# Kernel optimization log

Measured on AMD Instinct MI355X. Metric: run time of the kernel, lower is better.

The kernel has to match this reference:

```python
import jax, jax.numpy as jnp
import numpy as np

VIEW, NDET = 360, 736
H = W = 320
SCD, SDD = 500.0, 1000.0
DET_INT, REC_INT = 1.0, 1.1
NPOW2 = int(2 ** np.ceil(np.log2(2 * NDET - 1)))  # 2048
D_BETA = np.pi * 360.0 / VIEW / 180.0
DELTA_S = SCD / SDD * DET_INT


def _geometry():
    beta = np.linspace(0.0, (VIEW - 1) * D_BETA, VIEW)
    s_range = SCD / SDD * DET_INT * np.linspace((1 - NDET) / 2, (NDET - 1) / 2, NDET)
    cos_weight = np.cos(np.arctan2(s_range, SCD))
    # Ram-Lak spatial filter over offsets -(N-1)..(N-1), zero-padded to NPOW2, in freq domain
    n = np.arange(NPOW2) - (NDET - 1)
    h = np.zeros(NPOW2)
    h[n == 0] = 1.0 / (4.0 * DELTA_S ** 2)
    odd = (n % 2) != 0
    h[odd] = -1.0 / (np.pi * n[odd] * DELTA_S) ** 2
    recon_filter = np.real(np.fft.fft(h))[None, :]   # [1, NPOW2]
    window = np.ones((1, NPOW2))
    # backprojection sampling grid (fan-beam, equally spaced detector)
    x = REC_INT * np.linspace((1 - H) / 2, (H - 1) / 2, H)
    y = REC_INT * np.linspace((1 - W) / 2, (W - 1) / 2, W)
    x_mat, y_mat = np.meshgrid(x, y, indexing='xy')
    r = np.sqrt(x_mat ** 2 + y_mat ** 2)
    phi = np.arctan2(y_mat, x_mat)
    U = (SCD + r[None] * np.sin(beta[:, None, None] - phi[None])) / SCD
    s_xy = r[None] * np.cos(beta[:, None, None] - phi[None]) / U
    s_xy_n = (s_xy / s_range[-1]).reshape(VIEW, -1)
    view_xy_n = np.tile(np.linspace(-1.0, 1.0, VIEW)[:, None], [1, H * W])
    grid = np.stack([s_xy_n, view_xy_n], axis=2)     # [V, P, 2]
    square = (U ** 2).reshape(VIEW, -1)              # [V, P]
    # circular FOV mask
    gamma_e = np.arctan2(DET_INT * (NDET - 1) / 2, SDD)
    radius = SCD * np.sin(gamma_e) / REC_INT
    xg, yg = np.meshgrid(np.linspace(-(H - 1) / 2, (H - 1) / 2, H),
                         np.linspace(-(W - 1) / 2, (W - 1) / 2, W), indexing='xy')
    mask = ((((xg / radius) ** 2 + (yg / radius) ** 2) ** 2) < 1).astype(np.float32)
    return cos_weight, recon_filter, window, grid, square, mask


def setup_inputs() -> dict:
    key = jax.random.key(0)
    cw, rf, win, grid, square, mask = _geometry()
    f32 = lambda a: jnp.asarray(a, jnp.float32)
    return {
        "sinogram": jax.random.normal(key, (1, 1, VIEW, NDET), jnp.float32),
        "cos_weight": f32(cw), "recon_filter": f32(rf), "window": f32(win),
        "grid": f32(grid), "square": f32(square), "mask": f32(mask),
    }


def reference(sinogram, cos_weight, recon_filter, window, grid, square, mask):
    B, C, V, N = sinogram.shape
    Hh, Ww = mask.shape
    # FFT ramp filtering of cosine-weighted sinogram
    S = jnp.fft.fft(sinogram * cos_weight[None, None, None, :],
                    n=recon_filter.shape[-1], axis=-1)
    S = S * (recon_filter * window)[None, None]
    filt = (DELTA_S * jnp.fft.ifft(S, axis=-1)).real[..., N - 1:2 * N - 1]  # [B,C,V,N]
    # grid_sample: mode='nearest', padding_mode='zeros', align_corners=False
    gx, gy = grid[..., 0], grid[..., 1]                  # [V, P]
    ix = jnp.round(((gx + 1.0) * N - 1.0) / 2.0).astype(jnp.int32)
    iy = jnp.round(((gy + 1.0) * V - 1.0) / 2.0).astype(jnp.int32)
    valid = (ix >= 0) & (ix < N) & (iy >= 0) & (iy < V)
    sampled = filt[:, :, jnp.clip(iy, 0, V - 1), jnp.clip(ix, 0, N - 1)]   # [B,C,V,P]
    sampled = jnp.where(valid[None, None], sampled, 0.0)
    # weighted view-sum backprojection
    recon = D_BETA * jnp.sum(sampled / square[None, None], axis=2)         # [B,C,P]
    return recon.reshape(B, C, Hh, Ww) * mask[None, None]
```

## Files before the change

kernel.cpp:

```cpp
#include <hip/hip_runtime.h>

#define VIEWN 360
#define NDETC 736
#define HWPIX 102400
#define VC    8
#define VPC   45
#define NWORK 66240
#define FBLK  518

#define OFF_FILT 0
#define OFF_PART 1059840
#define OFF_DTAB 4336640
#define OFF_IY   4342400

__global__ __launch_bounds__(256) void filter_tab_kernel(
    const float* __restrict__ sino, const float* __restrict__ cw,
    const float* __restrict__ grid, char* __restrict__ ws)
{
    const int tid = threadIdx.x;
    if (blockIdx.x == FBLK) {
        double* dtab = (double*)(ws + OFF_DTAB);
        int*    iyt  = (int*)   (ws + OFF_IY);
        for (int v = tid; v < VIEWN; v += 256) {
            const double db   = ((3.141592653589793 * 360.0) / 360.0) / 180.0;
            const double stop = 359.0 * db;
            const double step = stop / 359.0;
            const double beta = (v == 359) ? stop : (double)v * step;
            dtab[2 * v]     = sin(beta);
            dtab[2 * v + 1] = cos(beta);
            const float gy = grid[(size_t)v * HWPIX * 2 + 1];
            float t = __fadd_rn(gy, 1.f);
            t = __fmul_rn(t, 360.f);
            t = __fadd_rn(t, -1.f);
            t = __fmul_rn(t, 0.5f);
            iyt[v] = __float2int_rn(t);
        }
        return;
    }
    __shared__ __align__(16) float gs[1472];
    __shared__ __align__(16) float ws2[2][NDETC];
    __shared__ __align__(16) float comb[128][4];
    float* filt = (float*)(ws + OFF_FILT);
    const int b = blockIdx.x;
    const int vbase = (b * 128) / 184;
    for (int m = tid; m < 1472; m += 256) {
        const int n1 = m - 735;
        const int n2 = ((2048 - m) & 2047) - 735;
        const double h1 = (n1 == 0) ? 1.0 : ((n1 & 1) ? -4.0 / (9.869604401089358 * (double)(n1 * n1)) : 0.0);
        const double h2 = (n2 == 0) ? 1.0 : ((n2 & 1) ? -4.0 / (9.869604401089358 * (double)(n2 * n2)) : 0.0);
        gs[m] = (float)(0.25 * (h1 + h2));
    }
    for (int idx = tid; idx < 2 * NDETC; idx += 256) {
        const int vv = idx / NDETC, k = idx % NDETC;
        const int v = vbase + vv;
        if (v < VIEWN) ws2[vv][k] = sino[v * NDETC + k] * cw[k];
    }
    __syncthreads();
    const int o    = b * 128 + (tid & 127);
    const int half = tid >> 7;
    float4 acc = make_float4(0.f, 0.f, 0.f, 0.f);
    int v = 0, d = 0;
    if (o < NWORK) {
        v = o / 184;
        d = 4 * (o % 184);
        const float* wsrow = ws2[v - vbase];
        const int kbeg = 368 * half;
        float4 p = *(const float4*)&gs[d + 736 - kbeg];
        for (int k0 = kbeg; k0 < kbeg + 368; k0 += 4) {
            const float4 c = *(const float4*)&gs[d + 732 - k0];
            const float4 w = *(const float4*)&wsrow[k0];
            acc.x = fmaf(w.x, c.w, acc.x);
            acc.y = fmaf(w.x, p.x, acc.y);
            acc.z = fmaf(w.x, p.y, acc.z);
            acc.w = fmaf(w.x, p.z, acc.w);
            acc.x = fmaf(w.y, c.z, acc.x);
            acc.y = fmaf(w.y, c.w, acc.y);
            acc.z = fmaf(w.y, p.x, acc.z);
            acc.w = fmaf(w.y, p.y, acc.w);
            acc.x = fmaf(w.z, c.y, acc.x);
            acc.y = fmaf(w.z, c.z, acc.y);
            acc.z = fmaf(w.z, c.w, acc.z);
            acc.w = fmaf(w.z, p.x, acc.w);
            acc.x = fmaf(w.w, c.x, acc.x);
            acc.y = fmaf(w.w, c.y, acc.y);
            acc.z = fmaf(w.w, c.z, acc.z);
            acc.w = fmaf(w.w, c.w, acc.w);
            p = c;
        }
    }
    if (half == 1) *(float4*)&comb[tid & 127][0] = acc;
    __syncthreads();
    if (half == 0 && o < NWORK) {
        const float4 bs = *(const float4*)&comb[tid][0];
        acc.x += bs.x; acc.y += bs.y; acc.z += bs.z; acc.w += bs.w;
        *(float4*)&filt[v * NDETC + d] = acc;
    }
}

__global__ __launch_bounds__(256) void bp_kernel(
    char* __restrict__ ws, float* __restrict__ part_out)
{
    const float*  filt = (const float*)(ws + OFF_FILT);
    const double* dtab = (const double*)(ws + OFF_DTAB);
    const int*    iyt  = (const int*)(ws + OFF_IY);
    const int pb = blockIdx.x, c = blockIdx.y;
    const int p  = pb * 256 + threadIdx.x;
    const int j  = p % 320, i = p / 320;
    const double xj = ((double)j - 159.5) * 1.1;
    const double yi = ((double)i - 159.5) * 1.1;
    const double CGX = 500.0 / 183.75;
    const double INV = 1.0 / 250000.0;
    float acc = 0.f;
    const int v0 = c * VPC;
    #pragma unroll 3
    for (int v = v0; v < v0 + VPC; ++v) {
        const double sb = dtab[2 * v];
        const double cb = dtab[2 * v + 1];
        const int iy = iyt[v];
        const double rs  = sb * xj - cb * yi;
        const double num = cb * xj + sb * yi;
        const double t   = 500.0 + rs;
        double r0 = (double)__builtin_amdgcn_rcpf((float)t);
        r0 = r0 * fma(-t, r0, 2.0);
        r0 = r0 * fma(-t, r0, 2.0);
        const double gxd = (num * CGX) * r0;
        const float  gx  = (float)gxd;
        float tx = __fadd_rn(gx, 1.f);
        tx = __fmul_rn(tx, 736.f);
        tx = __fadd_rn(tx, -1.f);
        tx = __fmul_rn(tx, 0.5f);
        const int ix = __float2int_rn(tx);
        const bool valid = (ix >= 0) & (ix < NDETC) & (iy >= 0) & (iy < VIEWN);
        const int ixc = min(max(ix, 0), NDETC - 1);
        const int iyc = min(max(iy, 0), VIEWN - 1);
        const float val = valid ? filt[iyc * NDETC + ixc] : 0.f;
        const float sq  = (float)(t * t * INV);
        acc += val * __builtin_amdgcn_rcpf(sq);
    }
    part_out[(size_t)c * HWPIX + p] = acc;
}

__global__ __launch_bounds__(256) void reduce_kernel(
    const float* __restrict__ part, const float* __restrict__ mask,
    float* __restrict__ out)
{
    const int p = blockIdx.x * 256 + threadIdx.x;
    const double db = ((3.141592653589793 * 360.0) / 360.0) / 180.0;
    float s = 0.f;
    #pragma unroll
    for (int cc = 0; cc < VC; ++cc)
        s += part[(size_t)cc * HWPIX + p];
    out[p] = (float)(db * (double)s * (double)mask[p]);
}

extern "C" void kernel_launch(void* const* d_in, const int* in_sizes, int n_in,
                              void* d_out, int out_size, void* d_ws, size_t ws_size,
                              hipStream_t stream)
{
    (void)in_sizes; (void)n_in; (void)out_size; (void)ws_size;
    const float* sino = (const float*)d_in[0];
    const float* cw   = (const float*)d_in[1];
    const float* grid = (const float*)d_in[4];
    const float* mask = (const float*)d_in[6];
    float* out = (float*)d_out;
    char*  ws  = (char*)d_ws;
    float* part = (float*)(ws + OFF_PART);

    filter_tab_kernel<<<FBLK + 1, 256, 0, stream>>>(sino, cw, grid, ws);
    bp_kernel<<<dim3(HWPIX / 256, VC), 256, 0, stream>>>(ws, part);
    reduce_kernel<<<HWPIX / 256, 256, 0, stream>>>(part, mask, out);
}
```

Measured before the change: 61.07 us.

## Compute backprojection coordinates in fp32 with wavefront-level fp64 fallback near rounding ties

The backprojection loop now computes the detector coordinate in fp32 from precomputed float sin/cos tables, including versions pre-scaled by the geometry constant. If any lane lands within a small margin of a rounding tie, the whole wavefront recomputes in fp64 so the nearest-neighbour index still matches the reference. The distance weight is derived from the fp32 reciprocal, views with an invalid row index are skipped, and the unroll factor changes. This targets the slow fp64 arithmetic, at the cost of a divergent fallback branch and slightly different fp32 weights.

```diff
diff --git a/kernel.cpp b/kernel.cpp
--- a/kernel.cpp
+++ b/kernel.cpp
@@ -11,7 +11,8 @@
 #define OFF_FILT 0
 #define OFF_PART 1059840
 #define OFF_DTAB 4336640
-#define OFF_IY   4342400
+#define OFF_FTAB 4348160
+#define OFF_IY   4353920
 
 __global__ __launch_bounds__(256) void filter_tab_kernel(
     const float* __restrict__ sino, const float* __restrict__ cw,
@@ -20,14 +21,18 @@
     const int tid = threadIdx.x;
     if (blockIdx.x == FBLK) {
         double* dtab = (double*)(ws + OFF_DTAB);
+        float*  ftab = (float*) (ws + OFF_FTAB);
         int*    iyt  = (int*)   (ws + OFF_IY);
         for (int v = tid; v < VIEWN; v += 256) {
             const double db   = ((3.141592653589793 * 360.0) / 360.0) / 180.0;
             const double stop = 359.0 * db;
             const double step = stop / 359.0;
             const double beta = (v == 359) ? stop : (double)v * step;
-            dtab[2 * v]     = sin(beta);
-            dtab[2 * v + 1] = cos(beta);
+            const double sb = sin(beta), cb = cos(beta);
+            const double CGX = 500.0 / 183.75;
+            dtab[4*v] = sb; dtab[4*v+1] = cb; dtab[4*v+2] = cb*CGX; dtab[4*v+3] = sb*CGX;
+            ftab[4*v] = (float)sb; ftab[4*v+1] = (float)cb;
+            ftab[4*v+2] = (float)(cb*CGX); ftab[4*v+3] = (float)(sb*CGX);
             const float gy = grid[(size_t)v * HWPIX * 2 + 1];
             float t = __fadd_rn(gy, 1.f);
             t = __fmul_rn(t, 360.f);
@@ -102,40 +107,49 @@
 {
     const float*  filt = (const float*)(ws + OFF_FILT);
     const double* dtab = (const double*)(ws + OFF_DTAB);
+    const float*  ftab = (const float*)(ws + OFF_FTAB);
     const int*    iyt  = (const int*)(ws + OFF_IY);
     const int pb = blockIdx.x, c = blockIdx.y;
     const int p  = pb * 256 + threadIdx.x;
     const int j  = p % 320, i = p / 320;
-    const double xj = ((double)j - 159.5) * 1.1;
-    const double yi = ((double)i - 159.5) * 1.1;
-    const double CGX = 500.0 / 183.75;
-    const double INV = 1.0 / 250000.0;
+    const float  xjf = ((float)j - 159.5f) * 1.1f;
+    const float  yif = ((float)i - 159.5f) * 1.1f;
+    const double xj  = ((double)j - 159.5) * 1.1;
+    const double yi  = ((double)i - 159.5) * 1.1;
     float acc = 0.f;
     const int v0 = c * VPC;
-    #pragma unroll 3
+    #pragma unroll 5
     for (int v = v0; v < v0 + VPC; ++v) {
-        const double sb = dtab[2 * v];
-        const double cb = dtab[2 * v + 1];
         const int iy = iyt[v];
-        const double rs  = sb * xj - cb * yi;
-        const double num = cb * xj + sb * yi;
-        const double t   = 500.0 + rs;
-        double r0 = (double)__builtin_amdgcn_rcpf((float)t);
-        r0 = r0 * fma(-t, r0, 2.0);
-        r0 = r0 * fma(-t, r0, 2.0);
-        const double gxd = (num * CGX) * r0;
-        const float  gx  = (float)gxd;
-        float tx = __fadd_rn(gx, 1.f);
+        if ((unsigned)iy >= 360u) continue;
+        const float sbf = ftab[4*v], cbf = ftab[4*v+1];
+        const float cbCf = ftab[4*v+2], sbCf = ftab[4*v+3];
+        const float t = fmaf(sbf, xjf, fmaf(-cbf, yif, 500.f));
+        const float r = __builtin_amdgcn_rcpf(t);
+        const float numC = fmaf(cbCf, xjf, sbCf * yif);
+        float tx = __fadd_rn(numC * r, 1.f);
         tx = __fmul_rn(tx, 736.f);
         tx = __fadd_rn(tx, -1.f);
         tx = __fmul_rn(tx, 0.5f);
+        const float dd = fabsf(tx - rintf(tx));
+        if (__any(dd > 0.499f)) {
+            const double sb = dtab[4*v], cb = dtab[4*v+1];
+            const double cbC = dtab[4*v+2], sbC = dtab[4*v+3];
+            const double td = fma(sb, xj, 500.0 - cb * yi);
+            double r0 = (double)__builtin_amdgcn_rcpf((float)td);
+            r0 = r0 * fma(-td, r0, 2.0);
+            r0 = r0 * fma(-td, r0, 2.0);
+            const double gxd = fma(cbC, xj, sbC * yi) * r0;
+            float txx = __fadd_rn((float)gxd, 1.f);
+            txx = __fmul_rn(txx, 736.f);
+            txx = __fadd_rn(txx, -1.f);
+            txx = __fmul_rn(txx, 0.5f);
+            tx = txx;
+        }
         const int ix = __float2int_rn(tx);
-        const bool valid = (ix >= 0) & (ix < NDETC) & (iy >= 0) & (iy < VIEWN);
-        const int ixc = min(max(ix, 0), NDETC - 1);
-        const int iyc = min(max(iy, 0), VIEWN - 1);
-        const float val = valid ? filt[iyc * NDETC + ixc] : 0.f;
-        const float sq  = (float)(t * t * INV);
-        acc += val * __builtin_amdgcn_rcpf(sq);
+        const float w = 250000.f * r * r;
+        const float val = ((unsigned)ix < 736u) ? filt[iy * NDETC + ix] : 0.f;
+        acc = fmaf(val, w, acc);
     }
     part_out[(size_t)c * HWPIX + p] = acc;
 }
```

Result: slower. 65.09 us (+6.6%).
